# Performance work log

Hardware: AMD Instinct MI355X
Metric: run time of the kernel (lower is better)

## Reference

```python
import jax, jax.numpy as jnp
import numpy as np

N_NODES = 100000
N_EDGES = 1600000
D_IN = 64
D_OUT = 64


def setup_inputs() -> dict:
    key = jax.random.key(0)
    k1, k2, k3 = jax.random.split(key, 3)
    edge_index = jax.random.randint(k1, (2, N_EDGES), 0, N_NODES, dtype=jnp.int64)
    x = jax.random.normal(k2, (N_NODES, D_IN), dtype=jnp.float32)
    W = jax.random.normal(k3, (D_OUT, D_IN), dtype=jnp.float32) * (1.0 / np.sqrt(D_IN))
    return {"edge_index": edge_index, "x": x, "W": W}


def reference(edge_index, x, W):
    # GCN forward: h = W x, then out = D^{-1/2} A D^{-1/2} h (symmetric normalization
    # of the COO edge list, matching normalize_edge_index + CSR SpMM in the original).
    N = x.shape[0]
    row, col = edge_index[0], edge_index[1]
    # degree from row occurrences of the adjacency
    deg = jax.ops.segment_sum(jnp.ones(row.shape, x.dtype), row, num_segments=N)
    dinv_sqrt = jnp.where(deg > 0, 1.0 / jnp.sqrt(deg), 0.0)
    w = dinv_sqrt[row] * dinv_sqrt[col]  # [E] edge weights
    xh = x @ W.T                          # dense linear, bias=False  [N, D_OUT]
    # SpMM: out[r] = sum_e w_e * xh[col_e] for edges with row_e == r
    out = jax.ops.segment_sum(w[:, None] * xh[col], row, num_segments=N)
    return out
```

## Files before the change

kernel.cpp:

```cpp
#include <hip/hip_runtime.h>
#include <hip/hip_fp16.h>

#define D     64
#define RPB   256
#define BCAP  4608
#define EPB   4096
#define NBMAX 400

typedef __attribute__((ext_vector_type(8))) _Float16 f16x8;
typedef __attribute__((ext_vector_type(4))) float    f32x4;

__global__ __launch_bounds__(512) void bucket_kernel(const int* __restrict__ ei, int E,
                                                     int nb,
                                                     int* __restrict__ cursor,
                                                     int* __restrict__ bbuf) {
    __shared__ int hist[NBMAX];
    __shared__ int base_l[NBMAX];
    int tid = threadIdx.x;

    for (int i = tid; i < nb; i += 512) hist[i] = 0;
    __syncthreads();

    int e0 = blockIdx.x * EPB;
    int n  = min(EPB, E - e0);

    for (int idx = tid; idx < n; idx += 512)
        atomicAdd(&hist[ei[e0 + idx] >> 8], 1);
    __syncthreads();

    for (int i = tid; i < nb; i += 512) {
        int c = hist[i];
        base_l[i] = (c > 0) ? atomicAdd(&cursor[i], c) : 0;
        hist[i] = 0;
    }
    __syncthreads();

    for (int idx = tid; idx < n; idx += 512) {
        int r = ei[e0 + idx];
        int c = ei[E + e0 + idx];
        int b = r >> 8;
        int off = base_l[b] + atomicAdd(&hist[b], 1);
        if (off < BCAP)
            bbuf[(size_t)b * BCAP + off] = ((r & (RPB - 1)) << 17) | c;
    }
}

__global__ __launch_bounds__(512) void sort_kernel(const int* __restrict__ cursor,
                                                   int* __restrict__ bbuf,
                                                   float* __restrict__ dinv,
                                                   int4* __restrict__ rowinfo, int N) {
    __shared__ int sorted[BCAP];
    __shared__ int hist[RPB];
    __shared__ int curs[RPB];
    __shared__ int wsum[4];
    int b = blockIdx.x, tid = threadIdx.x;
    int cnt = min(cursor[b], BCAP);
    int* gbuf = bbuf + (size_t)b * BCAP;

    if (tid < RPB) hist[tid] = 0;
    __syncthreads();
    for (int j = tid; j < cnt; j += 512) atomicAdd(&hist[gbuf[j] >> 17], 1);
    __syncthreads();

    int dv = 0, s = 0;
    if (tid < RPB) {
        dv = hist[tid];
        s = dv;
#pragma unroll
        for (int off = 1; off < 64; off <<= 1) {
            int t = __shfl_up(s, off);
            if ((tid & 63) >= off) s += t;
        }
        if ((tid & 63) == 63) wsum[tid >> 6] = s;
    }
    __syncthreads();
    if (tid < RPB) {
        int woff = 0;
#pragma unroll
        for (int i = 0; i < 3; ++i)
            if ((tid >> 6) > i) woff += wsum[i];
        int excl = s + woff - dv;
        int r = (b << 8) + tid;
        if (r < N) {
            float di = (dv > 0) ? rsqrtf((float)dv) : 0.0f;
            dinv[r] = di;
            rowinfo[r] = make_int4(b * BCAP + excl, dv, __float_as_int(di), 0);
        }
        curs[tid] = excl;
    }
    __syncthreads();

    for (int j = tid; j < cnt; j += 512) {
        int v = gbuf[j];
        int pos = atomicAdd(&curs[v >> 17], 1);
        sorted[pos] = v;
    }
    __syncthreads();
    for (int j = tid; j < cnt; j += 512) gbuf[j] = sorted[j];
}

__global__ __launch_bounds__(256) void linear_kernel(const float* __restrict__ x,
                                                     const float* __restrict__ W,
                                                     const float* __restrict__ dinv,
                                                     __half* __restrict__ xh, int M) {
    int tid  = threadIdx.x;
    int lane = tid & 63;
    int wv   = tid >> 6;
    int r16  = lane & 15;
    int quad = lane >> 4;

    if (blockIdx.x == 0 && tid < D) xh[(size_t)M * D + tid] = __float2half(0.0f);

    f16x8 Bf[4][2];
#pragma unroll
    for (int g = 0; g < 4; ++g)
#pragma unroll
        for (int s = 0; s < 2; ++s) {
            const float4* wp = (const float4*)(W + (size_t)(16 * g + r16) * D + 32 * s + quad * 8);
            float4 w0 = wp[0], w1 = wp[1];
            f16x8 h;
            h[0] = (_Float16)w0.x; h[1] = (_Float16)w0.y;
            h[2] = (_Float16)w0.z; h[3] = (_Float16)w0.w;
            h[4] = (_Float16)w1.x; h[5] = (_Float16)w1.y;
            h[6] = (_Float16)w1.z; h[7] = (_Float16)w1.w;
            Bf[g][s] = h;
        }

    int ntiles = (M + 15) / 16;
    int stride = gridDim.x * 4;
    for (int t = blockIdx.x * 4 + wv; t < ntiles; t += stride) {
        int r0 = t * 16;
        int ra = min(r0 + r16, M - 1);
        const float4* xp = (const float4*)(x + (size_t)ra * D + quad * 8);
        float4 a0 = xp[0], a1 = xp[1], a2 = xp[8], a3 = xp[9];
        f16x8 A0, A1;
        A0[0] = (_Float16)a0.x; A0[1] = (_Float16)a0.y; A0[2] = (_Float16)a0.z; A0[3] = (_Float16)a0.w;
        A0[4] = (_Float16)a1.x; A0[5] = (_Float16)a1.y; A0[6] = (_Float16)a1.z; A0[7] = (_Float16)a1.w;
        A1[0] = (_Float16)a2.x; A1[1] = (_Float16)a2.y; A1[2] = (_Float16)a2.z; A1[3] = (_Float16)a2.w;
        A1[4] = (_Float16)a3.x; A1[5] = (_Float16)a3.y; A1[6] = (_Float16)a3.z; A1[7] = (_Float16)a3.w;

        f32x4 acc[4];
#pragma unroll
        for (int g = 0; g < 4; ++g) {
            f32x4 z = {0.f, 0.f, 0.f, 0.f};
            z = __builtin_amdgcn_mfma_f32_16x16x32_f16(A0, Bf[g][0], z, 0, 0, 0);
            acc[g] = __builtin_amdgcn_mfma_f32_16x16x32_f16(A1, Bf[g][1], z, 0, 0, 0);
        }

#pragma unroll
        for (int reg = 0; reg < 4; ++reg) {
            int rr = r0 + quad * 4 + reg;
            if (rr < M) {
                float dvr = dinv[rr];
                __half* op = xh + (size_t)rr * D + r16;
#pragma unroll
                for (int g = 0; g < 4; ++g)
                    op[16 * g] = __float2half(dvr * acc[g][reg]);
            }
        }
    }
}

__global__ __launch_bounds__(256) void spmm_kernel(const int4* __restrict__ rowinfo,
                                                   const int* __restrict__ bbuf,
                                                   const __half2* __restrict__ xh2,
                                                   float2* __restrict__ out2,
                                                   int N, int stride) {
    int wid = (blockIdx.x * 256 + threadIdx.x) >> 6;
    int c   = threadIdx.x & 63;
    int sub = c >> 5;
    int f   = c & 31;

    int r0 = wid;
    if (r0 >= N) return;

    int4 ri0 = rowinfo[r0];
    int4 ri1 = (r0 + stride < N) ? rowinfo[r0 + stride] : make_int4(0, 0, 0, 0);
    int  cn0 = (c < min(ri0.y, 64)) ? (bbuf[ri0.x + c] & 0x1FFFF) : N;

    for (int r = r0; r < N; r += stride) {
        int rn  = r + stride;
        int rn2 = rn + stride;
        int4 ri2 = (rn2 < N) ? rowinfo[rn2] : make_int4(0, 0, 0, 0);
        int  cn1 = (rn < N && c < min(ri1.y, 64)) ? (bbuf[ri1.x + c] & 0x1FFFF) : N;

        int   d  = ri0.y;
        float dr = __int_as_float(ri0.z);
        float ax = 0.f, ay = 0.f;

        int n = min(d, 64);
        int n16 = (n + 15) & ~15;
        for (int k = 0; k < n16; k += 16) {
            int e0 = __shfl(cn0, k +  0 + sub);
            int e1 = __shfl(cn0, k +  2 + sub);
            int e2 = __shfl(cn0, k +  4 + sub);
            int e3 = __shfl(cn0, k +  6 + sub);
            int e4 = __shfl(cn0, k +  8 + sub);
            int e5 = __shfl(cn0, k + 10 + sub);
            int e6 = __shfl(cn0, k + 12 + sub);
            int e7 = __shfl(cn0, k + 14 + sub);
            float2 v0 = __half22float2(xh2[(size_t)e0 * 32 + f]);
            float2 v1 = __half22float2(xh2[(size_t)e1 * 32 + f]);
            float2 v2 = __half22float2(xh2[(size_t)e2 * 32 + f]);
            float2 v3 = __half22float2(xh2[(size_t)e3 * 32 + f]);
            float2 v4 = __half22float2(xh2[(size_t)e4 * 32 + f]);
            float2 v5 = __half22float2(xh2[(size_t)e5 * 32 + f]);
            float2 v6 = __half22float2(xh2[(size_t)e6 * 32 + f]);
            float2 v7 = __half22float2(xh2[(size_t)e7 * 32 + f]);
            ax += ((v0.x + v1.x) + (v2.x + v3.x)) + ((v4.x + v5.x) + (v6.x + v7.x));
            ay += ((v0.y + v1.y) + (v2.y + v3.y)) + ((v4.y + v5.y) + (v6.y + v7.y));
        }
        for (int j0 = 64; j0 < d; j0 += 64) {
            int nn = min(d - j0, 64);
            int cnx = (c < nn) ? (bbuf[ri0.x + j0 + c] & 0x1FFFF) : N;
            int m16 = (nn + 15) & ~15;
            for (int k = 0; k < m16; k += 16) {
                int e0 = __shfl(cnx, k +  0 + sub);
                int e1 = __shfl(cnx, k +  2 + sub);
                int e2 = __shfl(cnx, k +  4 + sub);
                int e3 = __shfl(cnx, k +  6 + sub);
                int e4 = __shfl(cnx, k +  8 + sub);
                int e5 = __shfl(cnx, k + 10 + sub);
                int e6 = __shfl(cnx, k + 12 + sub);
                int e7 = __shfl(cnx, k + 14 + sub);
                float2 v0 = __half22float2(xh2[(size_t)e0 * 32 + f]);
                float2 v1 = __half22float2(xh2[(size_t)e1 * 32 + f]);
                float2 v2 = __half22float2(xh2[(size_t)e2 * 32 + f]);
                float2 v3 = __half22float2(xh2[(size_t)e3 * 32 + f]);
                float2 v4 = __half22float2(xh2[(size_t)e4 * 32 + f]);
                float2 v5 = __half22float2(xh2[(size_t)e5 * 32 + f]);
                float2 v6 = __half22float2(xh2[(size_t)e6 * 32 + f]);
                float2 v7 = __half22float2(xh2[(size_t)e7 * 32 + f]);
                ax += ((v0.x + v1.x) + (v2.x + v3.x)) + ((v4.x + v5.x) + (v6.x + v7.x));
                ay += ((v0.y + v1.y) + (v2.y + v3.y)) + ((v4.y + v5.y) + (v6.y + v7.y));
            }
        }

        float sx = ax + __shfl(ax, c ^ 32);
        float sy = ay + __shfl(ay, c ^ 32);
        if (sub == 0) {
            float2 res = make_float2(dr * sx, dr * sy);
            __builtin_nontemporal_store(__builtin_bit_cast(double, res),
                                        (double*)&out2[(size_t)r * 32 + f]);
        }
        ri0 = ri1; ri1 = ri2; cn0 = cn1;
    }
}

extern "C" void kernel_launch(void* const* d_in, const int* in_sizes, int n_in,
                              void* d_out, int out_size, void* d_ws, size_t ws_size,
                              hipStream_t stream) {
    const int*   ei = (const int*)d_in[0];
    const float* x  = (const float*)d_in[1];
    const float* W  = (const float*)d_in[2];
    float* out = (float*)d_out;

    int E  = in_sizes[0] / 2;
    int N  = in_sizes[1] / D;
    int nb = (N + RPB - 1) / RPB;

    char* p = (char*)d_ws;
    size_t off = 0;
    auto take = [&](size_t bytes) -> char* {
        char* cur = p + off;
        off = (off + bytes + 255) & ~(size_t)255;
        return cur;
    };
    float*  dinv    = (float*)take((size_t)N * 4);
    int4*   rowinfo = (int4*)take((size_t)N * 16);
    int*    cursor  = (int*)take((size_t)nb * 4);
    int*    bbuf    = (int*)take((size_t)nb * BCAP * 4);
    __half* xh      = (__half*)take((size_t)(N + 1) * D * 2);
    (void)ws_size;

    hipMemsetAsync(cursor, 0, (size_t)nb * 4, stream);

    bucket_kernel<<<(E + EPB - 1) / EPB, 512, 0, stream>>>(ei, E, nb, cursor, bbuf);
    sort_kernel<<<nb, 512, 0, stream>>>(cursor, bbuf, dinv, rowinfo, N);
    linear_kernel<<<1024, 256, 0, stream>>>(x, W, dinv, xh, N);

    int spmm_blocks = 3072;
    spmm_kernel<<<spmm_blocks, 256, 0, stream>>>(rowinfo, bbuf, (const __half2*)xh,
                                                 (float2*)out, N, spmm_blocks * 4);
}
```

Before: 167.8 us.

## Fuse per-bucket sort with dense linear transform, vectorize bucket loads

Merges the sort kernel and the MFMA linear kernel into one kernel. Each 256-row bucket block computes its rows' degree scaling into shared memory, then transforms those same rows of x with W. This removes a kernel launch and the global dinv round trip. Bucket reads and writes in the sort now use int4 vector accesses. The trade-off is that the linear work runs on only about 391 blocks of 512 threads, not a 1024-block grid-stride launch, and the larger per-block register and LDS footprint may reduce occupancy.

```diff
diff --git a/kernel.cpp b/kernel.cpp
--- a/kernel.cpp
+++ b/kernel.cpp
@@ -45,21 +45,31 @@
     }
 }
 
-__global__ __launch_bounds__(512) void sort_kernel(const int* __restrict__ cursor,
-                                                   int* __restrict__ bbuf,
-                                                   float* __restrict__ dinv,
-                                                   int4* __restrict__ rowinfo, int N) {
-    __shared__ int sorted[BCAP];
-    __shared__ int hist[RPB];
-    __shared__ int curs[RPB];
-    __shared__ int wsum[4];
+__global__ __launch_bounds__(512) void sort_linear_kernel(const int* __restrict__ cursor,
+                                                          int* __restrict__ bbuf,
+                                                          const float* __restrict__ x,
+                                                          const float* __restrict__ W,
+                                                          int4* __restrict__ rowinfo,
+                                                          __half* __restrict__ xh, int N) {
+    __shared__ int   sorted[BCAP];
+    __shared__ int   hist[RPB];
+    __shared__ int   curs[RPB];
+    __shared__ float sdinv[RPB];
+    __shared__ int   wsum[4];
     int b = blockIdx.x, tid = threadIdx.x;
     int cnt = min(cursor[b], BCAP);
     int* gbuf = bbuf + (size_t)b * BCAP;
 
     if (tid < RPB) hist[tid] = 0;
     __syncthreads();
-    for (int j = tid; j < cnt; j += 512) atomicAdd(&hist[gbuf[j] >> 17], 1);
+
+    for (int j = tid * 4; j < cnt; j += 2048) {
+        int4 v = *(const int4*)(gbuf + j);
+        atomicAdd(&hist[(v.x >> 17) & 255], 1);
+        if (j + 1 < cnt) atomicAdd(&hist[(v.y >> 17) & 255], 1);
+        if (j + 2 < cnt) atomicAdd(&hist[(v.z >> 17) & 255], 1);
+        if (j + 3 < cnt) atomicAdd(&hist[(v.w >> 17) & 255], 1);
+    }
     __syncthreads();
 
     int dv = 0, s = 0;
@@ -80,57 +90,54 @@
         for (int i = 0; i < 3; ++i)
             if ((tid >> 6) > i) woff += wsum[i];
         int excl = s + woff - dv;
+        float di = (dv > 0) ? rsqrtf((float)dv) : 0.0f;
+        sdinv[tid] = di;
         int r = (b << 8) + tid;
-        if (r < N) {
-            float di = (dv > 0) ? rsqrtf((float)dv) : 0.0f;
-            dinv[r] = di;
+        if (r < N)
             rowinfo[r] = make_int4(b * BCAP + excl, dv, __float_as_int(di), 0);
-        }
         curs[tid] = excl;
     }
     __syncthreads();
 
-    for (int j = tid; j < cnt; j += 512) {
-        int v = gbuf[j];
-        int pos = atomicAdd(&curs[v >> 17], 1);
-        sorted[pos] = v;
-    }
-    __syncthreads();
-    for (int j = tid; j < cnt; j += 512) gbuf[j] = sorted[j];
-}
-
-__global__ __launch_bounds__(256) void linear_kernel(const float* __restrict__ x,
-                                                     const float* __restrict__ W,
-                                                     const float* __restrict__ dinv,
-                                                     __half* __restrict__ xh, int M) {
-    int tid  = threadIdx.x;
+    for (int j = tid * 4; j < cnt; j += 2048) {
+        int4 v = *(const int4*)(gbuf + j);
+        sorted[atomicAdd(&curs[(v.x >> 17) & 255], 1)] = v.x;
+        if (j + 1 < cnt) sorted[atomicAdd(&curs[(v.y >> 17) & 255], 1)] = v.y;
+        if (j + 2 < cnt) sorted[atomicAdd(&curs[(v.z >> 17) & 255], 1)] = v.z;
+        if (j + 3 < cnt) sorted[atomicAdd(&curs[(v.w >> 17) & 255], 1)] = v.w;
+    }
+    __syncthreads();
+
+    int cnt4 = (cnt + 3) & ~3;
+    for (int j = tid * 4; j < cnt4; j += 2048)
+        *(int4*)(gbuf + j) = *(const int4*)(sorted + j);
+
     int lane = tid & 63;
     int wv   = tid >> 6;
     int r16  = lane & 15;
     int quad = lane >> 4;
 
-    if (blockIdx.x == 0 && tid < D) xh[(size_t)M * D + tid] = __float2half(0.0f);
+    if (b == 0 && tid < D) xh[(size_t)N * D + tid] = __float2half(0.0f);
 
     f16x8 Bf[4][2];
 #pragma unroll
     for (int g = 0; g < 4; ++g)
 #pragma unroll
-        for (int s = 0; s < 2; ++s) {
-            const float4* wp = (const float4*)(W + (size_t)(16 * g + r16) * D + 32 * s + quad * 8);
+        for (int s2 = 0; s2 < 2; ++s2) {
+            const float4* wp = (const float4*)(W + (size_t)(16 * g + r16) * D + 32 * s2 + quad * 8);
             float4 w0 = wp[0], w1 = wp[1];
             f16x8 h;
             h[0] = (_Float16)w0.x; h[1] = (_Float16)w0.y;
             h[2] = (_Float16)w0.z; h[3] = (_Float16)w0.w;
             h[4] = (_Float16)w1.x; h[5] = (_Float16)w1.y;
             h[6] = (_Float16)w1.z; h[7] = (_Float16)w1.w;
-            Bf[g][s] = h;
-        }
-
-    int ntiles = (M + 15) / 16;
-    int stride = gridDim.x * 4;
-    for (int t = blockIdx.x * 4 + wv; t < ntiles; t += stride) {
-        int r0 = t * 16;
-        int ra = min(r0 + r16, M - 1);
+            Bf[g][s2] = h;
+        }
+
+    for (int tl = wv; tl < 16; tl += 8) {
+        int r0 = (b << 8) + tl * 16;
+        if (r0 >= N) break;
+        int ra = min(r0 + r16, N - 1);
         const float4* xp = (const float4*)(x + (size_t)ra * D + quad * 8);
         float4 a0 = xp[0], a1 = xp[1], a2 = xp[8], a3 = xp[9];
         f16x8 A0, A1;
@@ -149,9 +156,10 @@
 
 #pragma unroll
         for (int reg = 0; reg < 4; ++reg) {
-            int rr = r0 + quad * 4 + reg;
-            if (rr < M) {
-                float dvr = dinv[rr];
+            int rl = tl * 16 + quad * 4 + reg;
+            int rr = (b << 8) + rl;
+            if (rr < N) {
+                float dvr = sdinv[rl];
                 __half* op = xh + (size_t)rr * D + r16;
 #pragma unroll
                 for (int g = 0; g < 4; ++g)
@@ -266,7 +274,6 @@
         off = (off + bytes + 255) & ~(size_t)255;
         return cur;
     };
-    float*  dinv    = (float*)take((size_t)N * 4);
     int4*   rowinfo = (int4*)take((size_t)N * 16);
     int*    cursor  = (int*)take((size_t)nb * 4);
     int*    bbuf    = (int*)take((size_t)nb * BCAP * 4);
@@ -276,8 +283,7 @@
     hipMemsetAsync(cursor, 0, (size_t)nb * 4, stream);
 
     bucket_kernel<<<(E + EPB - 1) / EPB, 512, 0, stream>>>(ei, E, nb, cursor, bbuf);
-    sort_kernel<<<nb, 512, 0, stream>>>(cursor, bbuf, dinv, rowinfo, N);
-    linear_kernel<<<1024, 256, 0, stream>>>(x, W, dinv, xh, N);
+    sort_linear_kernel<<<nb, 512, 0, stream>>>(cursor, bbuf, x, W, rowinfo, xh, N);
 
     int spmm_blocks = 3072;
     spmm_kernel<<<spmm_blocks, 256, 0, stream>>>(rowinfo, bbuf, (const __half2*)xh,
```

New measurement: 160.7 us. 4.3% less time.
